# Performance work log

Measured on AMD Instinct MI355X. Metric: run time of the kernel, lower is better.

The kernel has to match this reference:

```python
import jax, jax.numpy as jnp
import numpy as np

DIM = 1024
NUM_HEADS = 16
HEAD_DIM = DIM // NUM_HEADS
ROPE_THETA = 10000.0
SCALE = HEAD_DIM ** -0.5


def _apply_rope(x, cos, sin):
    # x: [B, H, S, head_dim]; cos/sin: [S, head_dim//2] (broadcast over B, H)
    x_even = x[..., 0::2]
    x_odd = x[..., 1::2]
    rot_even = x_even * cos - x_odd * sin
    rot_odd = x_even * sin + x_odd * cos
    # interleave back: stack on last axis then flatten, matching torch .stack(-1).flatten(-2)
    return jnp.stack([rot_even, rot_odd], axis=-1).reshape(x.shape)


def setup_inputs() -> dict:
    key = jax.random.key(0)
    k0, k1, k2 = jax.random.split(key, 3)
    B, S = 2, 2048
    x = jax.random.normal(k0, (B, S, DIM), dtype=jnp.float32)
    # small_init: std = sqrt(2 / (5*dim))
    qkv_w = jax.random.normal(k1, (3 * DIM, DIM), dtype=jnp.float32) * (2.0 / (5 * DIM)) ** 0.5
    qkv_b = jnp.zeros((3 * DIM,), dtype=jnp.float32)
    # wang_init: std = 2 / num_blocks / sqrt(dim) scaled
    out_w = jax.random.normal(k2, (DIM, DIM), dtype=jnp.float32) * (2.0 / DIM) ** 0.5 / 2.0
    out_b = jnp.zeros((DIM,), dtype=jnp.float32)
    return {"x": x, "qkv_w": qkv_w, "qkv_b": qkv_b, "out_w": out_w, "out_b": out_b, "window_size": 512}


def reference(x, qkv_w, qkv_b, out_w, out_b, window_size):
    B, S, D = x.shape
    qkv = x @ qkv_w.T + qkv_b                          # [B, S, 3D]
    qkv = qkv.reshape(B, S, 3, NUM_HEADS, HEAD_DIM).transpose(2, 0, 3, 1, 4)
    q, k, v = qkv[0], qkv[1], qkv[2]                   # each [B, H, S, hd]

    pos = jnp.arange(S, dtype=jnp.float32)
    inv_freq = 1.0 / (ROPE_THETA ** (jnp.arange(0, HEAD_DIM, 2, dtype=jnp.float32) / HEAD_DIM))
    freqs = pos[:, None] * inv_freq                    # [S, hd//2]
    cos, sin = jnp.cos(freqs), jnp.sin(freqs)
    q = _apply_rope(q, cos, sin)
    k = _apply_rope(k, cos, sin)

    scores = jnp.einsum('bhqd,bhkd->bhqk', q, k) * SCALE
    i = jnp.arange(S)
    mask = (i[:, None] >= i[None, :]) & ((i[:, None] - i[None, :]) < window_size)  # causal sliding window
    scores = jnp.where(mask, scores, -jnp.inf)
    attn = jax.nn.softmax(scores, axis=-1)
    out = jnp.einsum('bhqk,bhkd->bhqd', attn, v)       # [B, H, S, hd]
    out = out.transpose(0, 2, 1, 3).reshape(B, S, D)
    return out @ out_w.T + out_b
```

## Files before the change

kernel.cpp:

```cpp
#include <hip/hip_runtime.h>
#include <hip/hip_bf16.h>
#include <cstdint>
#include <cstddef>

using bf16x8 = __attribute__((ext_vector_type(8))) short;
using f32x4  = __attribute__((ext_vector_type(4))) float;

#define MFMA16(a, b, c) __builtin_amdgcn_mfma_f32_16x16x32_bf16((a), (b), (c), 0, 0, 0)

__device__ __forceinline__ unsigned short f2bf(float f) {
    unsigned int u = __float_as_uint(f);
    u += 0x7fffu + ((u >> 16) & 1u);
    return (unsigned short)(u >> 16);
}
__device__ __forceinline__ uint32_t pack2bf(float a, float b) {
    __hip_bfloat162 h = __float22bfloat162_rn(float2{a, b});
    return *(uint32_t*)&h;
}
__device__ __forceinline__ float bf2f(short x) {
    return __uint_as_float(((uint32_t)(unsigned short)x) << 16);
}

__device__ __forceinline__ void gload_lds16(const void* g, void* l) {
    __builtin_amdgcn_global_load_lds(
        (const __attribute__((address_space(1))) void*)g,
        (__attribute__((address_space(3))) void*)l, 16, 0, 0);
}

#define S_LEN 2048
#define NHEAD 16
#define HDIM  64
#define DIM   1024
#define WIN   512
#define MROWS 4096

__global__ void prep(float* __restrict__ cosT, float* __restrict__ sinT,
                     const float* __restrict__ x, unsigned short* __restrict__ xb,
                     const float* __restrict__ qw, unsigned short* __restrict__ qwb,
                     const float* __restrict__ ow, unsigned short* __restrict__ owb) {
    int t = blockIdx.x * 256 + threadIdx.x;
    if (t < 65536) {
        int s = t >> 5, f = t & 31;
        float invf = powf(10000.0f, -(float)f / 32.0f);
        float ang = (float)s * invf;
        cosT[t] = cosf(ang);
        sinT[t] = sinf(ang);
        return;
    }
    int u = t - 65536;
    const float* src;
    unsigned short* dst;
    int i;
    if (u < 1048576)        { src = x;  dst = xb;  i = u * 4; }
    else if (u < 1835008)   { src = qw; dst = qwb; i = (u - 1048576) * 4; }
    else                    { src = ow; dst = owb; i = (u - 1835008) * 4; }
    float4 v = *(const float4*)(src + i);
    ushort4 o;
    o.x = f2bf(v.x); o.y = f2bf(v.y); o.z = f2bf(v.z); o.w = f2bf(v.w);
    *(ushort4*)(dst + i) = o;
}

__global__ __launch_bounds__(256) void gemm_qkv_fused(
        const unsigned short* __restrict__ A,
        const unsigned short* __restrict__ Bw,
        const float* __restrict__ bias,
        const float* __restrict__ cosT, const float* __restrict__ sinT,
        unsigned short* __restrict__ qbuf,
        unsigned short* __restrict__ kbuf,
        unsigned short* __restrict__ vtb) {
    __shared__ __align__(16) char smem_raw[34816];
    const int tid = threadIdx.x;
    const int lane = tid & 63, w = tid >> 6;
    const int wr = w >> 1, wc = w & 1, lm = lane & 15, lg = lane >> 4;
    const int lin = blockIdx.y * 24 + blockIdx.x;
    const int Lr = (lin & 7) * 96 + (lin >> 3);
    const int bx = Lr % 24, by = Lr / 24;
    const int row0 = by * 128, col0 = bx * 128;
    const int plane = bx >> 3;
    const int h0 = (bx & 7) * 2;
    const int b = by >> 4, s_base = (by & 15) * 128;

    f32x4 acc[4][4];
#pragma unroll
    for (int m = 0; m < 4; ++m)
#pragma unroll
        for (int n = 0; n < 4; ++n) acc[m][n] = (f32x4){0.f, 0.f, 0.f, 0.f};

    short* As = (short*)smem_raw;
    short* Bs = (short*)(smem_raw + 16384);

    for (int kt = 0; kt < 16; ++kt) {
#pragma unroll
        for (int i = 0; i < 4; ++i) {
            int c = tid + 256 * i;
            int r = c >> 3, gs = (c & 7) ^ (r & 7);
            gload_lds16((const char*)A  + (size_t)(row0 + r) * 2048 + (size_t)kt * 128 + gs * 16, As + c * 8);
            gload_lds16((const char*)Bw + (size_t)(col0 + r) * 2048 + (size_t)kt * 128 + gs * 16, Bs + c * 8);
        }
        __syncthreads();
        bf16x8 af0[4], af1[4], bf0[4], bf1[4];
#pragma unroll
        for (int m = 0; m < 4; ++m) {
            int rl = wr * 64 + m * 16 + lm, rb = rl & 7;
            af0[m] = *(const bf16x8*)&As[rl * 64 + ((lg ^ rb) << 3)];
            af1[m] = *(const bf16x8*)&As[rl * 64 + (((lg + 4) ^ rb) << 3)];
        }
#pragma unroll
        for (int n = 0; n < 4; ++n) {
            int rl = wc * 64 + n * 16 + lm, rb = rl & 7;
            bf0[n] = *(const bf16x8*)&Bs[rl * 64 + ((lg ^ rb) << 3)];
            bf1[n] = *(const bf16x8*)&Bs[rl * 64 + (((lg + 4) ^ rb) << 3)];
        }
#pragma unroll
        for (int m = 0; m < 4; ++m)
#pragma unroll
            for (int n = 0; n < 4; ++n) {
                acc[m][n] = MFMA16(af0[m], bf0[n], acc[m][n]);
                acc[m][n] = MFMA16(af1[m], bf1[n], acc[m][n]);
            }
        __syncthreads();
    }

    unsigned short (*tile)[136] = (unsigned short(*)[136])smem_raw;
    const int lane8 = tid & 7, idx = tid >> 3;

    if (plane < 2) {
#pragma unroll
        for (int m = 0; m < 4; ++m)
#pragma unroll
            for (int n = 0; n < 4; ++n) {
                int colL = wc * 64 + n * 16 + lm;
                float bv = bias[col0 + colL];
#pragma unroll
                for (int r = 0; r < 4; ++r)
                    tile[wr * 64 + m * 16 + lg * 4 + r][colL] = f2bf(acc[m][n][r] + bv);
            }
    } else {
#pragma unroll
        for (int m = 0; m < 4; ++m)
#pragma unroll
            for (int n = 0; n < 4; ++n) {
                int colL = wc * 64 + n * 16 + lm;
                float bv = bias[col0 + colL];
                uint2 pk;
                pk.x = pack2bf(acc[m][n][0] + bv, acc[m][n][1] + bv);
                pk.y = pack2bf(acc[m][n][2] + bv, acc[m][n][3] + bv);
                *(uint2*)&tile[colL][wr * 64 + m * 16 + lg * 4] = pk;
            }
    }
    __syncthreads();

    if (plane < 2) {
        unsigned short* dstp = (plane == 0) ? qbuf : kbuf;
        const float qsc = (plane == 0) ? 0.125f : 1.0f;
        int d0 = lane8 * 8;
#pragma unroll
        for (int j = 0; j < 4; ++j) {
            int srow = idx + 32 * j;
            int s = s_base + srow;
            float4 c4 = *(const float4*)&cosT[s * 32 + (d0 >> 1)];
            float4 s4 = *(const float4*)&sinT[s * 32 + (d0 >> 1)];
#pragma unroll
            for (int hh = 0; hh < 2; ++hh) {
                bf16x8 v = *(const bf16x8*)&tile[srow][hh * 64 + d0];
                float e0 = bf2f(v[0]), o0 = bf2f(v[1]);
                float e1 = bf2f(v[2]), o1 = bf2f(v[3]);
                float e2 = bf2f(v[4]), o2 = bf2f(v[5]);
                float e3 = bf2f(v[6]), o3 = bf2f(v[7]);
                uint4 pk;
                pk.x = pack2bf((e0 * c4.x - o0 * s4.x) * qsc, (e0 * s4.x + o0 * c4.x) * qsc);
                pk.y = pack2bf((e1 * c4.y - o1 * s4.y) * qsc, (e1 * s4.y + o1 * c4.y) * qsc);
                pk.z = pack2bf((e2 * c4.z - o2 * s4.z) * qsc, (e2 * s4.z + o2 * c4.z) * qsc);
                pk.w = pack2bf((e3 * c4.w - o3 * s4.w) * qsc, (e3 * s4.w + o3 * c4.w) * qsc);
                int h = h0 + hh;
                *(uint4*)&dstp[(((size_t)(b * NHEAD + h)) * S_LEN + s) * 64 + d0] = pk;
            }
        }
    } else {
#pragma unroll
        for (int rr = 0; rr < 4; ++rr) {
            int hd = rr * 32 + idx;
            int hh = hd >> 6, d = hd & 63, h = h0 + hh;
#pragma unroll
            for (int j = 0; j < 2; ++j) {
                int s0 = lane8 * 8 + j * 64;
                bf16x8 v = *(const bf16x8*)&tile[hd][s0];
                *(bf16x8*)&vtb[((size_t)(b * NHEAD + h) * 64 + d) * S_LEN +
                               s_base + s0] = v;
            }
        }
    }
}

__global__ __launch_bounds__(256) void gemm_out(const unsigned short* __restrict__ A,
                                                const unsigned short* __restrict__ Bw,
                                                const float* __restrict__ bias,
                                                float* __restrict__ Cout) {
    __shared__ __align__(16) char smem_raw[24576];
    const int tid = threadIdx.x;
    const int lane = tid & 63, w = tid >> 6;
    const int wr = w >> 1, wc = w & 1, lm = lane & 15, lg = lane >> 4;
    const int lin = blockIdx.y * 16 + blockIdx.x;
    const int Lr = (lin & 7) * 64 + (lin >> 3);
    const int bx = Lr & 15, by = Lr >> 4;
    const int row0 = by * 128, col0 = bx * 64;

    f32x4 acc[4][2];
#pragma unroll
    for (int m = 0; m < 4; ++m)
#pragma unroll
        for (int n = 0; n < 2; ++n) acc[m][n] = (f32x4){0.f, 0.f, 0.f, 0.f};

    short* As = (short*)smem_raw;
    short* Bs = (short*)(smem_raw + 16384);

    for (int kt = 0; kt < 16; ++kt) {
#pragma unroll
        for (int i = 0; i < 4; ++i) {
            int c = tid + 256 * i;
            int r = c >> 3, gs = (c & 7) ^ (r & 7);
            gload_lds16((const char*)A + (size_t)(row0 + r) * 2048 + (size_t)kt * 128 + gs * 16, As + c * 8);
        }
#pragma unroll
        for (int i = 0; i < 2; ++i) {
            int c = tid + 256 * i;
            int r = c >> 3, gs = (c & 7) ^ (r & 7);
            gload_lds16((const char*)Bw + (size_t)(col0 + r) * 2048 + (size_t)kt * 128 + gs * 16, Bs + c * 8);
        }
        __syncthreads();
        bf16x8 af0[4], af1[4], bf0[2], bf1[2];
#pragma unroll
        for (int m = 0; m < 4; ++m) {
            int rl = wr * 64 + m * 16 + lm, rb = rl & 7;
            af0[m] = *(const bf16x8*)&As[rl * 64 + ((lg ^ rb) << 3)];
            af1[m] = *(const bf16x8*)&As[rl * 64 + (((lg + 4) ^ rb) << 3)];
        }
#pragma unroll
        for (int n = 0; n < 2; ++n) {
            int rl = wc * 32 + n * 16 + lm, rb = rl & 7;
            bf0[n] = *(const bf16x8*)&Bs[rl * 64 + ((lg ^ rb) << 3)];
            bf1[n] = *(const bf16x8*)&Bs[rl * 64 + (((lg + 4) ^ rb) << 3)];
        }
#pragma unroll
        for (int m = 0; m < 4; ++m)
#pragma unroll
            for (int n = 0; n < 2; ++n) {
                acc[m][n] = MFMA16(af0[m], bf0[n], acc[m][n]);
                acc[m][n] = MFMA16(af1[m], bf1[n], acc[m][n]);
            }
        __syncthreads();
    }

#pragma unroll
    for (int m = 0; m < 4; ++m) {
        int row = row0 + wr * 64 + m * 16 + lg * 4;
#pragma unroll
        for (int n = 0; n < 2; ++n) {
            int col = col0 + wc * 32 + n * 16 + lm;
            float bv = bias[col];
#pragma unroll
            for (int r = 0; r < 4; ++r)
                Cout[(size_t)(row + r) * DIM + col] = acc[m][n][r] + bv;
        }
    }
}

__global__ __launch_bounds__(256) void attn(const unsigned short* __restrict__ qb,
                                            const unsigned short* __restrict__ kb,
                                            const unsigned short* __restrict__ vt,
                                            unsigned short* __restrict__ ao) {
    const int p = blockIdx.x;
    const int L = (p & 7) * 128 + (p >> 3);
    const int qblk = L & 31, bh = L >> 5;
    const int b = bh >> 4, h = bh & 15;
    const int tid = threadIdx.x, w = tid >> 6, lane = tid & 63;
    const int lm = lane & 15, lg = lane >> 4;
    const unsigned short* Qb = qb + (size_t)bh * S_LEN * 64;
    const unsigned short* Kb = kb + (size_t)bh * S_LEN * 64;
    const unsigned short* Vt = vt + (size_t)bh * 64 * S_LEN;
    const int q0 = qblk * 64 + w * 16;

    __shared__ short Ks[128 * 64];
    __shared__ short Vs[64 * 128];
    __shared__ short Plds[4][16 * 64];
    short* Pw = Plds[w];

    bf16x8 aq0 = *(const bf16x8*)&Qb[(q0 + lm) * 64 + lg * 8];
    bf16x8 aq1 = *(const bf16x8*)&Qb[(q0 + lm) * 64 + lg * 8 + 32];

    f32x4 o[4];
#pragma unroll
    for (int n = 0; n < 4; ++n) o[n] = (f32x4){0.f, 0.f, 0.f, 0.f};
    float lsum = 0.f;

    const int qq = q0 + lm;
    const int t0_64 = qblk >= 8 ? qblk - 8 : 0;
    const int first = t0_64 >> 1, last = qblk >> 1;
    const int sw = lm & 7;

    for (int kt = first; kt <= last; ++kt) {
#pragma unroll
        for (int i = 0; i < 4; ++i) {
            int c = tid + 256 * i;
            int r = c >> 3, g = (c & 7) ^ (r & 7);
            gload_lds16(Kb + (size_t)(kt * 128 + r) * 64 + g * 8, &Ks[c * 8]);
        }
#pragma unroll
        for (int i = 0; i < 4; ++i) {
            int c = tid + 256 * i;
            int r = c >> 4, g = (c & 15) ^ (r & 7);
            gload_lds16(Vt + (size_t)r * S_LEN + kt * 128 + g * 8, &Vs[c * 8]);
        }
        __syncthreads();
#pragma unroll
        for (int half = 0; half < 2; ++half) {
            const int h64 = kt * 2 + half;
            if (h64 < t0_64 || h64 > qblk) continue;
            const int kbase = h64 * 64;
            f32x4 sT[4];
            __builtin_amdgcn_s_setprio(1);
#pragma unroll
            for (int n = 0; n < 4; ++n) {
                int rl = half * 64 + n * 16 + lm;
                bf16x8 bk0 = *(const bf16x8*)&Ks[rl * 64 + ((lg ^ sw) << 3)];
                bf16x8 bk1 = *(const bf16x8*)&Ks[rl * 64 + (((lg + 4) ^ sw) << 3)];
                f32x4 z = (f32x4){0.f, 0.f, 0.f, 0.f};
                z = MFMA16(bk0, aq0, z);
                sT[n] = MFMA16(bk1, aq1, z);
            }
            __builtin_amdgcn_s_setprio(0);
#pragma unroll
            for (int n = 0; n < 4; ++n) {
                int kk0 = kbase + n * 16 + lg * 4;
#pragma unroll
                for (int r = 0; r < 4; ++r) {
                    int d = qq - (kk0 + r);
                    float pv = ((unsigned)d < (unsigned)WIN) ? __expf(sT[n][r]) : 0.f;
                    sT[n][r] = pv;
                    lsum += pv;
                }
                uint2 pk;
                pk.x = pack2bf(sT[n][0], sT[n][1]);
                pk.y = pack2bf(sT[n][2], sT[n][3]);
                *(uint2*)&Pw[lm * 64 + ((((2 * n + (lg >> 1)) ^ sw) << 3) + ((lg & 1) << 2))] = pk;
            }
            bf16x8 ap0 = *(const bf16x8*)&Pw[lm * 64 + ((lg ^ sw) << 3)];
            bf16x8 ap1 = *(const bf16x8*)&Pw[lm * 64 + (((lg + 4) ^ sw) << 3)];
            __builtin_amdgcn_s_setprio(1);
#pragma unroll
            for (int n = 0; n < 4; ++n) {
                int rl = n * 16 + lm;
                bf16x8 bv0 = *(const bf16x8*)&Vs[rl * 128 + half * 64 + ((lg ^ sw) << 3)];
                bf16x8 bv1 = *(const bf16x8*)&Vs[rl * 128 + half * 64 + (((lg + 4) ^ sw) << 3)];
                o[n] = MFMA16(ap0, bv0, o[n]);
                o[n] = MFMA16(ap1, bv1, o[n]);
            }
            __builtin_amdgcn_s_setprio(0);
        }
        __syncthreads();
    }
    lsum += __shfl_xor(lsum, 16, 64);
    lsum += __shfl_xor(lsum, 32, 64);
    float linv = 1.f / lsum;
    float lrow[4];
#pragma unroll
    for (int r = 0; r < 4; ++r) lrow[r] = __shfl(linv, lg * 4 + r, 64);
#pragma unroll
    for (int n = 0; n < 4; ++n)
#pragma unroll
        for (int r = 0; r < 4; ++r) {
            int row = b * S_LEN + q0 + lg * 4 + r;
            int col = h * 64 + n * 16 + lm;
            ao[(size_t)row * DIM + col] = f2bf(o[n][r] * lrow[r]);
        }
}

extern "C" void kernel_launch(void* const* d_in, const int* in_sizes, int n_in,
                              void* d_out, int out_size, void* d_ws, size_t ws_size,
                              hipStream_t stream) {
    const float* x      = (const float*)d_in[0];
    const float* qkv_w  = (const float*)d_in[1];
    const float* qkv_b  = (const float*)d_in[2];
    const float* out_w  = (const float*)d_in[3];
    const float* out_b  = (const float*)d_in[4];
    (void)in_sizes; (void)n_in; (void)out_size; (void)ws_size;

    char* ws = (char*)d_ws;
    float*          cosT = (float*)(ws + 0);
    float*          sinT = (float*)(ws + 262144);
    unsigned short* xb   = (unsigned short*)(ws + 524288);
    unsigned short* wqb  = (unsigned short*)(ws + 8912896);
    unsigned short* owb  = (unsigned short*)(ws + 15204352);
    unsigned short* qbuf = (unsigned short*)(ws + 17301504);
    unsigned short* kbuf = (unsigned short*)(ws + 25690112);
    unsigned short* vtb  = (unsigned short*)(ws + 34078720);
    unsigned short* aob  = (unsigned short*)(ws + 42467328);

    prep<<<8448, 256, 0, stream>>>(cosT, sinT, x, xb, qkv_w, wqb, out_w, owb);

    gemm_qkv_fused<<<dim3(24, 32), 256, 0, stream>>>(xb, wqb, qkv_b, cosT, sinT,
                                                     qbuf, kbuf, vtb);

    attn<<<1024, 256, 0, stream>>>(qbuf, kbuf, vtb, aob);

    gemm_out<<<dim3(16, 32), 256, 0, stream>>>(aob, owb, out_b, (float*)d_out);
}
```

Before: 96.00 us.

## Specialize attention mask by tile type and drop GEMM block swizzle

The attention inner loop now classifies each 64-key tile as interior, diagonal, or window-edge. Interior tiles skip per-element mask tests, while the other two use a simpler one-sided comparison. Separately, both GEMM kernels drop the remapping of block indices to tiles and use blockIdx directly. That removes the L2-locality grouping, which may change cache reuse. The mask specialization adds branches and code size but removes integer compares and selects from the common case.

Result: slower. 99.11 us (+3.2%).

```diff
diff --git a/kernel.cpp b/kernel.cpp
--- a/kernel.cpp
+++ b/kernel.cpp
@@ -72,9 +72,7 @@
     const int tid = threadIdx.x;
     const int lane = tid & 63, w = tid >> 6;
     const int wr = w >> 1, wc = w & 1, lm = lane & 15, lg = lane >> 4;
-    const int lin = blockIdx.y * 24 + blockIdx.x;
-    const int Lr = (lin & 7) * 96 + (lin >> 3);
-    const int bx = Lr % 24, by = Lr / 24;
+    const int bx = blockIdx.x, by = blockIdx.y;
     const int row0 = by * 128, col0 = bx * 128;
     const int plane = bx >> 3;
     const int h0 = (bx & 7) * 2;
@@ -200,10 +198,7 @@
     const int tid = threadIdx.x;
     const int lane = tid & 63, w = tid >> 6;
     const int wr = w >> 1, wc = w & 1, lm = lane & 15, lg = lane >> 4;
-    const int lin = blockIdx.y * 16 + blockIdx.x;
-    const int Lr = (lin & 7) * 64 + (lin >> 3);
-    const int bx = Lr & 15, by = Lr >> 4;
-    const int row0 = by * 128, col0 = bx * 64;
+    const int row0 = blockIdx.y * 128, col0 = blockIdx.x * 64;
 
     f32x4 acc[4][2];
 #pragma unroll
@@ -317,6 +312,7 @@
             const int h64 = kt * 2 + half;
             if (h64 < t0_64 || h64 > qblk) continue;
             const int kbase = h64 * 64;
+            const int mode = (h64 == qblk) ? 1 : ((qblk >= 8 && h64 == t0_64) ? 2 : 0);
             f32x4 sT[4];
             __builtin_amdgcn_s_setprio(1);
 #pragma unroll
@@ -329,16 +325,40 @@
                 sT[n] = MFMA16(bk1, aq1, z);
             }
             __builtin_amdgcn_s_setprio(0);
-#pragma unroll
-            for (int n = 0; n < 4; ++n) {
-                int kk0 = kbase + n * 16 + lg * 4;
-#pragma unroll
-                for (int r = 0; r < 4; ++r) {
-                    int d = qq - (kk0 + r);
-                    float pv = ((unsigned)d < (unsigned)WIN) ? __expf(sT[n][r]) : 0.f;
-                    sT[n][r] = pv;
-                    lsum += pv;
+            if (mode == 0) {
+#pragma unroll
+                for (int n = 0; n < 4; ++n)
+#pragma unroll
+                    for (int r = 0; r < 4; ++r) {
+                        float pv = __expf(sT[n][r]);
+                        sT[n][r] = pv;
+                        lsum += pv;
+                    }
+            } else if (mode == 1) {
+#pragma unroll
+                for (int n = 0; n < 4; ++n) {
+                    int kk0 = kbase + n * 16 + lg * 4;
+#pragma unroll
+                    for (int r = 0; r < 4; ++r) {
+                        float pv = (kk0 + r <= qq) ? __expf(sT[n][r]) : 0.f;
+                        sT[n][r] = pv;
+                        lsum += pv;
+                    }
                 }
+            } else {
+#pragma unroll
+                for (int n = 0; n < 4; ++n) {
+                    int kk0 = kbase + n * 16 + lg * 4;
+#pragma unroll
+                    for (int r = 0; r < 4; ++r) {
+                        float pv = (qq - (kk0 + r) < WIN) ? __expf(sT[n][r]) : 0.f;
+                        sT[n][r] = pv;
+                        lsum += pv;
+                    }
+                }
+            }
+#pragma unroll
+            for (int n = 0; n < 4; ++n) {
                 uint2 pk;
                 pk.x = pack2bf(sT[n][0], sT[n][1]);
                 pk.y = pack2bf(sT[n][2], sT[n][3]);
```
